# Optimization experiments

Hardware: AMD Instinct MI355X
Metric: run time of the kernel (lower is better)

Reference implementation:

```python
import jax, jax.numpy as jnp
import numpy as np
import math

B, C, L = 8, 64, 2048
H = 4            # num_heads
CH = C // H      # head channels = 16
G = max(1, C // 16)  # GroupNorm groups = 4
EPS = 1e-5


def setup_inputs() -> dict:
    key = jax.random.key(0)
    ks = jax.random.split(key, 4)
    x = jax.random.normal(ks[0], (B, C, L), dtype=jnp.float32)
    gn_w = jnp.ones((C,), jnp.float32)
    gn_b = jnp.zeros((C,), jnp.float32)
    qkv_w = jax.random.normal(ks[1], (3 * C, C), jnp.float32) / math.sqrt(C)
    qkv_b = jnp.zeros((3 * C,), jnp.float32)
    # note: original zero-inits proj_out; we use random weights for a non-trivial baseline
    proj_w = jax.random.normal(ks[2], (C, C), jnp.float32) / math.sqrt(C)
    proj_b = jnp.zeros((C,), jnp.float32)
    return {"x": x, "gn_w": gn_w, "gn_b": gn_b, "qkv_w": qkv_w,
            "qkv_b": qkv_b, "proj_w": proj_w, "proj_b": proj_b}


def _group_norm(x, w, b):
    # x: [B, C, L], groups over channel dim
    xg = x.reshape(B, G, (C // G) * L)
    mean = jnp.mean(xg, axis=-1, keepdims=True)
    var = jnp.var(xg, axis=-1, keepdims=True)
    xn = ((xg - mean) * jax.lax.rsqrt(var + EPS)).reshape(B, C, L)
    return xn * w[None, :, None] + b[None, :, None]


def reference(x, gn_w, gn_b, qkv_w, qkv_b, proj_w, proj_b):
    xn = _group_norm(x, gn_w, gn_b)
    # conv1x1 QKV: [B, 3C, L]
    qkv = jnp.einsum('oc,bcl->bol', qkv_w, xn) + qkv_b[None, :, None]
    q, k, v = jnp.split(qkv, 3, axis=1)            # each [B, C, L]
    q = q.reshape(B * H, CH, L)
    k = k.reshape(B * H, CH, L)
    v = v.reshape(B * H, CH, L)
    scale = 1.0 / math.sqrt(math.sqrt(CH))          # double-scaled as in source
    w = jnp.einsum('bct,bcs->bts', q * scale, k * scale)  # [B*H, L, L]
    w = jax.nn.softmax(w.astype(jnp.float32), axis=-1).astype(q.dtype)
    a = jnp.einsum('bts,bcs->bct', w, v).reshape(B, C, L)
    h = jnp.einsum('oc,bcl->bol', proj_w, a) + proj_b[None, :, None]
    return x + h
```

## Files before the change

### kernel.cpp

```cpp
#include <hip/hip_runtime.h>
#include <hip/hip_bf16.h>

#define LL 2048

typedef float f32x16 __attribute__((ext_vector_type(16)));
typedef float f32x4 __attribute__((ext_vector_type(4)));
typedef short short8 __attribute__((ext_vector_type(8)));

__device__ __forceinline__ float exp2_fast(float x) {
    float r;
    asm volatile("v_exp_f32 %0, %1" : "=v"(r) : "v"(x));
    return r;
}

__device__ __forceinline__ uint32_t pack2(float a, float b) {
    union { __hip_bfloat16 h; unsigned short s; } ua, ub;
    ua.h = __float2bfloat16(a);
    ub.h = __float2bfloat16(b);
    return (uint32_t)ua.s | ((uint32_t)ub.s << 16);
}

__device__ __forceinline__ unsigned short bf16of(float a) {
    union { __hip_bfloat16 h; unsigned short s; } u;
    u.h = __float2bfloat16(a);
    return u.s;
}

__global__ __launch_bounds__(256) void k_gnstats(const float* __restrict__ x,
                                                 float* __restrict__ stats) {
    int bg = blockIdx.x >> 2, part = blockIdx.x & 3;
    const f32x4* p = (const f32x4*)(x + (size_t)bg * (16 * LL)) + part * 2048;
    float s1 = 0.f, s2 = 0.f;
    for (int i = threadIdx.x; i < 2048; i += 256) {
        f32x4 v = p[i];
        s1 += v[0] + v[1] + v[2] + v[3];
        s2 += v[0] * v[0] + v[1] * v[1] + v[2] * v[2] + v[3] * v[3];
    }
#pragma unroll
    for (int off = 32; off > 0; off >>= 1) {
        s1 += __shfl_down(s1, off, 64);
        s2 += __shfl_down(s2, off, 64);
    }
    __shared__ float r1[4], r2[4];
    int lane = threadIdx.x & 63, wv = threadIdx.x >> 6;
    if (lane == 0) { r1[wv] = s1; r2[wv] = s2; }
    __syncthreads();
    if (threadIdx.x == 0) {
        atomicAdd(&stats[bg * 2],     r1[0] + r1[1] + r1[2] + r1[3]);
        atomicAdd(&stats[bg * 2 + 1], r2[0] + r2[1] + r2[2] + r2[3]);
    }
}

__global__ __launch_bounds__(256) void k_qkv(const float* __restrict__ x,
                                             const float* __restrict__ gnw,
                                             const float* __restrict__ gnb,
                                             const float* __restrict__ qw,
                                             const float* __restrict__ qb,
                                             const float* __restrict__ stats,
                                             unsigned short* __restrict__ qt,
                                             unsigned short* __restrict__ kt,
                                             unsigned short* __restrict__ vb) {
    int lt = blockIdx.x;
    int ot = blockIdx.y;
    int b  = blockIdx.z;
    int tid = threadIdx.x;
    int l0 = lt * 64;
    __shared__ unsigned short xs[64 * 64];
    __shared__ unsigned short ws[64 * 64];

#pragma unroll
    for (int k = 0; k < 4; k++) {
        int chunk = tid + k * 256;
        int c = chunk >> 4, l4 = chunk & 15;
        f32x4 v = *(const f32x4*)(x + ((size_t)b * 64 + c) * LL + l0 + l4 * 4);
        int g = c >> 4;
        float s1 = stats[(b * 4 + g) * 2], s2 = stats[(b * 4 + g) * 2 + 1];
        float mean = s1 * (1.0f / 32768.0f);
        float var  = s2 * (1.0f / 32768.0f) - mean * mean;
        float rstd = rsqrtf(var + 1e-5f);
        float wgt = gnw[c] * rstd;
        float bia = gnb[c] - mean * wgt;
#pragma unroll
        for (int j = 0; j < 4; j++) {
            int l = l4 * 4 + j;
            xs[l * 64 + (c ^ ((l & 7) << 3))] = bf16of(v[j] * wgt + bia);
        }
        int o = c, c4 = l4;
        f32x4 wv4 = *(const f32x4*)(qw + (size_t)(ot * 64 + o) * 64 + c4 * 4);
        uint2 pw2 = make_uint2(pack2(wv4[0], wv4[1]), pack2(wv4[2], wv4[3]));
        *(uint2*)&ws[o * 64 + ((c4 * 4) ^ ((o & 7) << 3))] = pw2;
    }
    __syncthreads();

    int wv_ = tid >> 6, lane = tid & 63, hi = lane >> 5, tl = lane & 31;
    int o0 = (wv_ & 1) * 32, lw = (wv_ >> 1) * 32;
    int arow = o0 + tl, brow = lw + tl;
    f32x16 acc = {};
#pragma unroll
    for (int kk = 0; kk < 4; kk++) {
        int cb = kk * 16 + hi * 8;
        short8 af = *(const short8*)&ws[arow * 64 + (cb ^ ((arow & 7) << 3))];
        short8 bf = *(const short8*)&xs[brow * 64 + (cb ^ ((brow & 7) << 3))];
        acc = __builtin_amdgcn_mfma_f32_32x32x16_bf16(af, bf, acc, 0, 0, 0);
    }

    int t = l0 + lw + tl;
    if (ot < 2) {
        float sc = ot ? 0.72134752f : 0.5f;
        unsigned short* base = (ot ? kt : qt) + (size_t)(b * 4) * (LL * 16);
#pragma unroll
        for (int g = 0; g < 4; g++) {
            int ob = o0 + 8 * g + 4 * hi;
            float v0 = (acc[4 * g]     + qb[ot * 64 + ob])     * sc;
            float v1 = (acc[4 * g + 1] + qb[ot * 64 + ob + 1]) * sc;
            float v2 = (acc[4 * g + 2] + qb[ot * 64 + ob + 2]) * sc;
            float v3 = (acc[4 * g + 3] + qb[ot * 64 + ob + 3]) * sc;
            uint2 pkv = make_uint2(pack2(v0, v1), pack2(v2, v3));
            *(uint2*)(base + (size_t)(ob >> 4) * (LL * 16) + (size_t)t * 16 + (ob & 15)) = pkv;
        }
    } else {
        unsigned short* base = vb + (size_t)(b * 4) * (16 * LL);
#pragma unroll
        for (int r = 0; r < 16; r++) {
            int o = o0 + (r & 3) + 8 * (r >> 2) + 4 * hi;
            base[(size_t)(o >> 4) * (16 * LL) + (size_t)(o & 15) * LL + t] =
                bf16of(acc[r] + qb[128 + o]);
        }
    }
}

__global__ __launch_bounds__(256) void k_attn(const unsigned short* __restrict__ qt,
                                              const unsigned short* __restrict__ kt,
                                              const unsigned short* __restrict__ vb,
                                              unsigned short* __restrict__ abuf) {
    int wv = threadIdx.x >> 6;
    int lane = threadIdx.x & 63;
    int hi = lane >> 5, tlo = lane & 31;
    int bh = blockIdx.y;
    int t0 = blockIdx.x * 32;

    __shared__ float lds_d2[3][32][17];
    __shared__ float lds_l[3][32];

    const unsigned short* qp = qt + (size_t)bh * (LL * 16);
    const unsigned short* kp = kt + (size_t)bh * (LL * 16);
    const unsigned short* vp = vb + (size_t)bh * (16 * LL) + (size_t)(tlo & 15) * LL;

    short8 qf = *(const short8*)(qp + (size_t)(t0 + tlo) * 16 + 8 * hi);

    f32x16 d2 = {};
    float lsum = 0.f;

    int sbeg = wv * 512;
    for (int s0 = sbeg; s0 < sbeg + 512; s0 += 32) {
        short8 kf  = *(const short8*)(kp + (size_t)(s0 + tlo) * 16 + 8 * hi);
        short8 vf0 = *(const short8*)(vp + s0 + 8 * hi);
        short8 vf1 = *(const short8*)(vp + s0 + 16 + 8 * hi);

        f32x16 z = {};
        f32x16 d1 = __builtin_amdgcn_mfma_f32_32x32x16_bf16(kf, qf, z, 0, 0, 0);

        float p[16], ps = 0.f;
#pragma unroll
        for (int r = 0; r < 16; r++) { p[r] = exp2_fast(d1[r]); ps += p[r]; }
        lsum += ps;

        uint32_t pk[8];
#pragma unroll
        for (int i = 0; i < 8; i++) pk[i] = pack2(p[2 * i], p[2 * i + 1]);

        uint32_t w0 = __shfl_xor(pk[0], 32, 64), w1 = __shfl_xor(pk[1], 32, 64);
        uint32_t w2 = __shfl_xor(pk[2], 32, 64), w3 = __shfl_xor(pk[3], 32, 64);
        uint32_t w4 = __shfl_xor(pk[4], 32, 64), w5 = __shfl_xor(pk[5], 32, 64);
        uint32_t w6 = __shfl_xor(pk[6], 32, 64), w7 = __shfl_xor(pk[7], 32, 64);
        union { uint32_t u[4]; short8 s; } A1, A2;
        A1.u[0] = hi ? w2 : pk[0];
        A1.u[1] = hi ? w3 : pk[1];
        A1.u[2] = hi ? pk[2] : w0;
        A1.u[3] = hi ? pk[3] : w1;
        A2.u[0] = hi ? w6 : pk[4];
        A2.u[1] = hi ? w7 : pk[5];
        A2.u[2] = hi ? pk[6] : w4;
        A2.u[3] = hi ? pk[7] : w5;

        d2 = __builtin_amdgcn_mfma_f32_32x32x16_bf16(A1.s, vf0, d2, 0, 0, 0);
        d2 = __builtin_amdgcn_mfma_f32_32x32x16_bf16(A2.s, vf1, d2, 0, 0, 0);
    }

    float ls = lsum + __shfl_xor(lsum, 32, 64);

    if (wv > 0) {
        int w = wv - 1;
#pragma unroll
        for (int r = 0; r < 16; r++) {
            int row = (r & 3) + 8 * (r >> 2) + 4 * hi;
            if (tlo < 16) lds_d2[w][row][tlo] = d2[r];
        }
        if (hi == 0) lds_l[w][tlo] = ls;
    }
    __syncthreads();
    if (wv == 0) {
        float lall = ls + lds_l[0][tlo] + lds_l[1][tlo] + lds_l[2][tlo];
        float rl = 1.0f / lall;
        int tc = tlo & 15;
        unsigned short* op = abuf + ((size_t)bh * 16 + tlo) * LL + t0;
        float v[16];
#pragma unroll
        for (int r = 0; r < 16; r++) {
            int row = (r & 3) + 8 * (r >> 2) + 4 * hi;
            float osum = d2[r] + lds_d2[0][row][tc]
                       + lds_d2[1][row][tc] + lds_d2[2][row][tc];
            v[r] = osum * __shfl(rl, row, 64);
        }
        if (tlo < 16) {
#pragma unroll
            for (int g = 0; g < 4; g++) {
                uint2 pkv = make_uint2(pack2(v[4 * g], v[4 * g + 1]),
                                       pack2(v[4 * g + 2], v[4 * g + 3]));
                *(uint2*)(op + 8 * g + 4 * hi) = pkv;
            }
        }
    }
}

__global__ __launch_bounds__(256) void k_proj(const float* __restrict__ x,
                                              const unsigned short* __restrict__ abuf,
                                              const float* __restrict__ pw,
                                              const float* __restrict__ pb,
                                              float* __restrict__ out) {
    int lt = blockIdx.x;
    int b  = blockIdx.y;
    int tid = threadIdx.x;
    int l0 = lt * 64;
    __shared__ unsigned short as_[64 * 64];
    __shared__ unsigned short ws[64 * 64];

#pragma unroll
    for (int k = 0; k < 2; k++) {
        int chunk = tid + k * 256;
        int c = chunk >> 3, l8 = chunk & 7;
        uint4 v8 = *(const uint4*)(abuf + (size_t)(b * 64 + c) * LL + l0 + l8 * 8);
        const unsigned short* sp = (const unsigned short*)&v8;
#pragma unroll
        for (int j = 0; j < 8; j++) {
            int l = l8 * 8 + j;
            as_[l * 64 + (c ^ ((l & 7) << 3))] = sp[j];
        }
    }
#pragma unroll
    for (int k = 0; k < 4; k++) {
        int chunk = tid + k * 256;
        int o = chunk >> 4, c4 = chunk & 15;
        f32x4 wv4 = *(const f32x4*)(pw + (size_t)o * 64 + c4 * 4);
        uint2 pw2 = make_uint2(pack2(wv4[0], wv4[1]), pack2(wv4[2], wv4[3]));
        *(uint2*)&ws[o * 64 + ((c4 * 4) ^ ((o & 7) << 3))] = pw2;
    }
    __syncthreads();

    int wv_ = tid >> 6, lane = tid & 63, hi = lane >> 5, tl = lane & 31;
    int o0 = (wv_ & 1) * 32, lw = (wv_ >> 1) * 32;
    int arow = o0 + tl, brow = lw + tl;
    f32x16 acc = {};
#pragma unroll
    for (int kk = 0; kk < 4; kk++) {
        int cb = kk * 16 + hi * 8;
        short8 af = *(const short8*)&ws[arow * 64 + (cb ^ ((arow & 7) << 3))];
        short8 bf = *(const short8*)&as_[brow * 64 + (cb ^ ((brow & 7) << 3))];
        acc = __builtin_amdgcn_mfma_f32_32x32x16_bf16(af, bf, acc, 0, 0, 0);
    }

    int l = l0 + lw + tl;
#pragma unroll
    for (int r = 0; r < 16; r++) {
        int o = o0 + (r & 3) + 8 * (r >> 2) + 4 * hi;
        size_t idx = (size_t)(b * 64 + o) * LL + l;
        out[idx] = x[idx] + acc[r] + pb[o];
    }
}

extern "C" void kernel_launch(void* const* d_in, const int* in_sizes, int n_in,
                              void* d_out, int out_size, void* d_ws, size_t ws_size,
                              hipStream_t stream) {
    const float* x   = (const float*)d_in[0];
    const float* gnw = (const float*)d_in[1];
    const float* gnb = (const float*)d_in[2];
    const float* qw  = (const float*)d_in[3];
    const float* qb  = (const float*)d_in[4];
    const float* pw  = (const float*)d_in[5];
    const float* pb  = (const float*)d_in[6];
    float* out = (float*)d_out;

    float* wsf   = (float*)d_ws;
    float* stats = wsf;
    unsigned short* qt = (unsigned short*)(wsf + 64);
    unsigned short* kt = qt + (size_t)32 * LL * 16;
    unsigned short* vb = kt + (size_t)32 * LL * 16;
    unsigned short* abuf = vb + (size_t)32 * LL * 16;

    hipMemsetAsync(stats, 0, 64 * sizeof(float), stream);
    hipLaunchKernelGGL(k_gnstats, dim3(128), dim3(256), 0, stream, x, stats);
    hipLaunchKernelGGL(k_qkv, dim3(32, 3, 8), dim3(256), 0, stream,
                       x, gnw, gnb, qw, qb, stats, qt, kt, vb);
    hipLaunchKernelGGL(k_attn, dim3(64, 32), dim3(256), 0, stream, qt, kt, vb, abuf);
    hipLaunchKernelGGL(k_proj, dim3(32, 8), dim3(256), 0, stream,
                       x, abuf, pw, pb, out);
}
```

Baseline: 125.7 us.

## Drop memset and atomics for GN stats; use permlane32 swap in attention

Each GroupNorm stats block now writes its partial sums to its own slot, and the QKV kernel adds the four partials itself. This removes the hipMemsetAsync launch and the atomic adds. In the attention inner loop, the eight cross-half shuffles plus selects are replaced by four v_permlane32_swap instructions that exchange register halves between the two 32-lane halves. The intent is less launch overhead and fewer instructions in the hot loop, at the cost of relying on gfx950-specific permlane semantics matching the old data layout.

```diff
diff --git a/kernel.cpp b/kernel.cpp
--- a/kernel.cpp
+++ b/kernel.cpp
@@ -24,6 +24,10 @@
     union { __hip_bfloat16 h; unsigned short s; } u;
     u.h = __float2bfloat16(a);
     return u.s;
+}
+
+__device__ __forceinline__ void permswap(uint32_t& d, uint32_t& s) {
+    asm("v_permlane32_swap_b32 %0, %1" : "+v"(d), "+v"(s));
 }
 
 __global__ __launch_bounds__(256) void k_gnstats(const float* __restrict__ x,
@@ -46,8 +50,8 @@
     if (lane == 0) { r1[wv] = s1; r2[wv] = s2; }
     __syncthreads();
     if (threadIdx.x == 0) {
-        atomicAdd(&stats[bg * 2],     r1[0] + r1[1] + r1[2] + r1[3]);
-        atomicAdd(&stats[bg * 2 + 1], r2[0] + r2[1] + r2[2] + r2[3]);
+        stats[blockIdx.x * 2]     = r1[0] + r1[1] + r1[2] + r1[3];
+        stats[blockIdx.x * 2 + 1] = r2[0] + r2[1] + r2[2] + r2[3];
     }
 }
 
@@ -74,7 +78,9 @@
         int c = chunk >> 4, l4 = chunk & 15;
         f32x4 v = *(const f32x4*)(x + ((size_t)b * 64 + c) * LL + l0 + l4 * 4);
         int g = c >> 4;
-        float s1 = stats[(b * 4 + g) * 2], s2 = stats[(b * 4 + g) * 2 + 1];
+        int sb = (b * 4 + g) * 8;
+        float s1 = stats[sb] + stats[sb + 2] + stats[sb + 4] + stats[sb + 6];
+        float s2 = stats[sb + 1] + stats[sb + 3] + stats[sb + 5] + stats[sb + 7];
         float mean = s1 * (1.0f / 32768.0f);
         float var  = s2 * (1.0f / 32768.0f) - mean * mean;
         float rstd = rsqrtf(var + 1e-5f);
@@ -169,19 +175,13 @@
 #pragma unroll
         for (int i = 0; i < 8; i++) pk[i] = pack2(p[2 * i], p[2 * i + 1]);
 
-        uint32_t w0 = __shfl_xor(pk[0], 32, 64), w1 = __shfl_xor(pk[1], 32, 64);
-        uint32_t w2 = __shfl_xor(pk[2], 32, 64), w3 = __shfl_xor(pk[3], 32, 64);
-        uint32_t w4 = __shfl_xor(pk[4], 32, 64), w5 = __shfl_xor(pk[5], 32, 64);
-        uint32_t w6 = __shfl_xor(pk[6], 32, 64), w7 = __shfl_xor(pk[7], 32, 64);
+        permswap(pk[0], pk[2]);
+        permswap(pk[1], pk[3]);
+        permswap(pk[4], pk[6]);
+        permswap(pk[5], pk[7]);
         union { uint32_t u[4]; short8 s; } A1, A2;
-        A1.u[0] = hi ? w2 : pk[0];
-        A1.u[1] = hi ? w3 : pk[1];
-        A1.u[2] = hi ? pk[2] : w0;
-        A1.u[3] = hi ? pk[3] : w1;
-        A2.u[0] = hi ? w6 : pk[4];
-        A2.u[1] = hi ? w7 : pk[5];
-        A2.u[2] = hi ? pk[6] : w4;
-        A2.u[3] = hi ? pk[7] : w5;
+        A1.u[0] = pk[0]; A1.u[1] = pk[1]; A1.u[2] = pk[2]; A1.u[3] = pk[3];
+        A2.u[0] = pk[4]; A2.u[1] = pk[5]; A2.u[2] = pk[6]; A2.u[3] = pk[7];
 
         d2 = __builtin_amdgcn_mfma_f32_32x32x16_bf16(A1.s, vf0, d2, 0, 0, 0);
         d2 = __builtin_amdgcn_mfma_f32_32x32x16_bf16(A2.s, vf1, d2, 0, 0, 0);
@@ -292,12 +292,11 @@
 
     float* wsf   = (float*)d_ws;
     float* stats = wsf;
-    unsigned short* qt = (unsigned short*)(wsf + 64);
+    unsigned short* qt = (unsigned short*)(wsf + 256);
     unsigned short* kt = qt + (size_t)32 * LL * 16;
     unsigned short* vb = kt + (size_t)32 * LL * 16;
     unsigned short* abuf = vb + (size_t)32 * LL * 16;
 
-    hipMemsetAsync(stats, 0, 64 * sizeof(float), stream);
     hipLaunchKernelGGL(k_gnstats, dim3(128), dim3(256), 0, stream, x, stats);
     hipLaunchKernelGGL(k_qkv, dim3(32, 3, 8), dim3(256), 0, stream,
                        x, gnw, gnb, qw, qb, stats, qt, kt, vb);
```

Result: no change. 124.9 us (-0.7%).
